# Kernel optimization log

Hardware: AMD Instinct MI355X
Metric: run time of the kernel (lower is better)

Reference implementation:

```python
import jax, jax.numpy as jnp
import numpy as np


def setup_inputs() -> dict:
    key = jax.random.key(0)
    k1, k2 = jax.random.split(key)
    STATE_LEN, SEQ_LEN, D = 8192, 8192, 1024
    user_emb = jax.random.normal(k1, (STATE_LEN, D), dtype=jnp.float32)
    id_emb = jax.random.normal(k2, (SEQ_LEN, D), dtype=jnp.float32)
    return {"user_emb": user_emb, "id_emb": id_emb}


def reference(user_emb, id_emb):
    # attn_energies[i, j] = user_emb[i] . id_emb[j]  -> single GEMM
    energies = jnp.einsum('id,jd->ij', user_emb, id_emb)  # [state_len, seq_len]
    # F.softmax on 2D tensor defaults to dim=1 (rows)
    return jax.nn.softmax(energies, axis=-1)
```

## Files before the change

### kernel.cpp

```cpp
#include <hip/hip_runtime.h>
#include <hip/hip_bf16.h>
#include <stdint.h>

typedef __attribute__((ext_vector_type(8))) short bf16x8;
typedef __attribute__((ext_vector_type(4))) float f32x4;

typedef const __attribute__((address_space(1))) void* gas_ptr;
typedef __attribute__((address_space(3))) void* lds_ptr_t;

__device__ __forceinline__ unsigned short f32_to_bf16_rtn(float x) {
    unsigned u = __float_as_uint(x);
    u += 0x7FFFu + ((u >> 16) & 1u);
    return (unsigned short)(u >> 16);
}
__device__ __forceinline__ float bf16_bits_to_f32(unsigned short h) {
    return __uint_as_float(((unsigned)h) << 16);
}

__global__ __launch_bounds__(256) void split_hi_lo(
    const float* __restrict__ A, const float* __restrict__ B,
    unsigned short* __restrict__ Ahi, unsigned short* __restrict__ Alo,
    unsigned short* __restrict__ Bhi, unsigned short* __restrict__ Blo, int n4)
{
    int i = blockIdx.x * 256 + threadIdx.x;
    if (i >= n4) return;
    float4 a = ((const float4*)A)[i];
    float4 b = ((const float4*)B)[i];
    ushort4 h, l;

    h.x = f32_to_bf16_rtn(a.x); l.x = f32_to_bf16_rtn(a.x - bf16_bits_to_f32(h.x));
    h.y = f32_to_bf16_rtn(a.y); l.y = f32_to_bf16_rtn(a.y - bf16_bits_to_f32(h.y));
    h.z = f32_to_bf16_rtn(a.z); l.z = f32_to_bf16_rtn(a.z - bf16_bits_to_f32(h.z));
    h.w = f32_to_bf16_rtn(a.w); l.w = f32_to_bf16_rtn(a.w - bf16_bits_to_f32(h.w));
    ((ushort4*)Ahi)[i] = h; ((ushort4*)Alo)[i] = l;

    h.x = f32_to_bf16_rtn(b.x); l.x = f32_to_bf16_rtn(b.x - bf16_bits_to_f32(h.x));
    h.y = f32_to_bf16_rtn(b.y); l.y = f32_to_bf16_rtn(b.y - bf16_bits_to_f32(h.y));
    h.z = f32_to_bf16_rtn(b.z); l.z = f32_to_bf16_rtn(b.z - bf16_bits_to_f32(h.z));
    h.w = f32_to_bf16_rtn(b.w); l.w = f32_to_bf16_rtn(b.w - bf16_bits_to_f32(h.w));
    ((ushort4*)Bhi)[i] = h; ((ushort4*)Blo)[i] = l;
}

template<int KC, int NC>
__global__ __launch_bounds__(256) void gemm_presplit(
    const __hip_bfloat16* __restrict__ Ahi, const __hip_bfloat16* __restrict__ Alo,
    const __hip_bfloat16* __restrict__ Bhi, const __hip_bfloat16* __restrict__ Blo,
    float* __restrict__ out, int M, int N, int K)
{
    const int Kd = (KC > 0) ? KC : K;
    const int Nd = (NC > 0) ? NC : N;

    __shared__ char sm[32768];
    const int tid  = threadIdx.x;
    const int lane = tid & 63;
    const int w    = tid >> 6;
    const int bm = blockIdx.y, bn = blockIdx.x;
    const int wm = (w >> 1) * 64;
    const int wn = (w & 1) * 64;

    f32x4 acc[4][4] = {};

    const int sfetch = (tid & 3) ^ ((tid >> 3) & 3);
    const size_t offA = (size_t)(bm * 128 + (tid >> 2)) * Kd + sfetch * 8;
    const size_t offB = (size_t)(bn * 128 + (tid >> 2)) * Kd + sfetch * 8;
    const __hip_bfloat16* pAh = Ahi + offA;
    const __hip_bfloat16* pAl = Alo + offA;
    const __hip_bfloat16* pBh = Bhi + offB;
    const __hip_bfloat16* pBl = Blo + offB;
    const size_t half = (size_t)64 * Kd;
    char* dst0 = sm + tid * 16;

    const int rA = lane & 15;
    const int ca = (lane >> 4) ^ ((lane >> 1) & 3);
    const char* aP = sm +         (wm + rA) * 64 + ca * 16;
    const char* bP = sm + 16384 + (wn + rA) * 64 + ca * 16;

#pragma unroll 4
    for (int k0 = 0; k0 < Kd; k0 += 32) {
        __syncthreads();
        __builtin_amdgcn_global_load_lds((gas_ptr)(pAh + k0),        (lds_ptr_t)(dst0),         16, 0, 0);
        __builtin_amdgcn_global_load_lds((gas_ptr)(pAh + half + k0), (lds_ptr_t)(dst0 + 4096),  16, 0, 0);
        __builtin_amdgcn_global_load_lds((gas_ptr)(pAl + k0),        (lds_ptr_t)(dst0 + 8192),  16, 0, 0);
        __builtin_amdgcn_global_load_lds((gas_ptr)(pAl + half + k0), (lds_ptr_t)(dst0 + 12288), 16, 0, 0);
        __builtin_amdgcn_global_load_lds((gas_ptr)(pBh + k0),        (lds_ptr_t)(dst0 + 16384), 16, 0, 0);
        __builtin_amdgcn_global_load_lds((gas_ptr)(pBh + half + k0), (lds_ptr_t)(dst0 + 20480), 16, 0, 0);
        __builtin_amdgcn_global_load_lds((gas_ptr)(pBl + k0),        (lds_ptr_t)(dst0 + 24576), 16, 0, 0);
        __builtin_amdgcn_global_load_lds((gas_ptr)(pBl + half + k0), (lds_ptr_t)(dst0 + 28672), 16, 0, 0);
        __syncthreads();

        bf16x8 bh[4], bl[4];
#pragma unroll
        for (int j = 0; j < 4; ++j) {
            bh[j] = *(const bf16x8*)(bP + j * 1024);
            bl[j] = *(const bf16x8*)(bP + j * 1024 + 8192);
        }
#pragma unroll
        for (int i = 0; i < 4; ++i) {
            bf16x8 ah = *(const bf16x8*)(aP + i * 1024);
            bf16x8 al = *(const bf16x8*)(aP + i * 1024 + 8192);
#pragma unroll
            for (int j = 0; j < 4; ++j) {
                acc[i][j] = __builtin_amdgcn_mfma_f32_16x16x32_bf16(ah, bh[j], acc[i][j], 0, 0, 0);
                acc[i][j] = __builtin_amdgcn_mfma_f32_16x16x32_bf16(al, bh[j], acc[i][j], 0, 0, 0);
                acc[i][j] = __builtin_amdgcn_mfma_f32_16x16x32_bf16(ah, bl[j], acc[i][j], 0, 0, 0);
            }
        }
    }

    const int r0 = bm * 128 + wm + ((lane >> 4) << 2);
    const int c0 = bn * 128 + wn + rA;
#pragma unroll
    for (int i = 0; i < 4; ++i)
#pragma unroll
        for (int j = 0; j < 4; ++j)
#pragma unroll
            for (int r = 0; r < 4; ++r)
                __builtin_nontemporal_store(
                    acc[i][j][r],
                    &out[(size_t)(r0 + i * 16 + r) * Nd + (c0 + j * 16)]);
}

__global__ __launch_bounds__(256) void gemm_fallback(
    const float* __restrict__ Af, const float* __restrict__ Bf,
    float* __restrict__ out, int M, int N, int K)
{
    __shared__ char sm[32768];
    const int tid  = threadIdx.x;
    const int lane = tid & 63;
    const int w    = tid >> 6;
    const int bm = blockIdx.y, bn = blockIdx.x;
    const int wm = (w >> 1) * 64;
    const int wn = (w & 1) * 64;

    f32x4 acc[4][4] = {};
    const int sfetch = (tid & 3) ^ ((tid >> 3) & 3);
    const int rA = lane & 15;
    const int ca = (lane >> 4) ^ ((lane >> 1) & 3);
    const char* aP = sm +         (wm + rA) * 64 + ca * 16;
    const char* bP = sm + 16384 + (wn + rA) * 64 + ca * 16;

    for (int k0 = 0; k0 < K; k0 += 32) {
        __syncthreads();
#pragma unroll
        for (int c = 0; c < 4; ++c) {
            const bool isA = (c < 2);
            const int row = ((c & 1) << 6) + (tid >> 2);
            const float* src = (isA ? Af + (size_t)(bm * 128 + row) * K
                                    : Bf + (size_t)(bn * 128 + row) * K)
                               + k0 + ((tid & 3) << 3);
            f32x4 v0 = *(const f32x4*)src;
            f32x4 v1 = *(const f32x4*)(src + 4);
            float vv[8] = {v0.x, v0.y, v0.z, v0.w, v1.x, v1.y, v1.z, v1.w};
            bf16x8 h, l;
#pragma unroll
            for (int j = 0; j < 8; ++j) {
                unsigned short hb = f32_to_bf16_rtn(vv[j]);
                unsigned short lb = f32_to_bf16_rtn(vv[j] - bf16_bits_to_f32(hb));
                h[j] = (short)hb; l[j] = (short)lb;
            }
            const int g = row * 64 + sfetch * 16;
            *(bf16x8*)(sm + (isA ? 0 : 16384) + g) = h;
            *(bf16x8*)(sm + (isA ? 8192 : 24576) + g) = l;
        }
        __syncthreads();

        bf16x8 bh[4], bl[4];
#pragma unroll
        for (int j = 0; j < 4; ++j) {
            bh[j] = *(const bf16x8*)(bP + j * 1024);
            bl[j] = *(const bf16x8*)(bP + j * 1024 + 8192);
        }
#pragma unroll
        for (int i = 0; i < 4; ++i) {
            bf16x8 ah = *(const bf16x8*)(aP + i * 1024);
            bf16x8 al = *(const bf16x8*)(aP + i * 1024 + 8192);
#pragma unroll
            for (int j = 0; j < 4; ++j) {
                acc[i][j] = __builtin_amdgcn_mfma_f32_16x16x32_bf16(ah, bh[j], acc[i][j], 0, 0, 0);
                acc[i][j] = __builtin_amdgcn_mfma_f32_16x16x32_bf16(al, bh[j], acc[i][j], 0, 0, 0);
                acc[i][j] = __builtin_amdgcn_mfma_f32_16x16x32_bf16(ah, bl[j], acc[i][j], 0, 0, 0);
            }
        }
    }

    const int r0 = bm * 128 + wm + ((lane >> 4) << 2);
    const int c0 = bn * 128 + wn + rA;
#pragma unroll
    for (int i = 0; i < 4; ++i)
#pragma unroll
        for (int j = 0; j < 4; ++j)
#pragma unroll
            for (int r = 0; r < 4; ++r)
                __builtin_nontemporal_store(
                    acc[i][j][r],
                    &out[(size_t)(r0 + i * 16 + r) * N + (c0 + j * 16)]);
}

__device__ __forceinline__ void lgkm_barrier()
{
    asm volatile("s_waitcnt lgkmcnt(0)" ::: "memory");
    __builtin_amdgcn_s_barrier();
    asm volatile("" ::: "memory");
}

__device__ __forceinline__ void softmax_row(
    f32x4 (&v)[8], f32x4 (&vn)[8], const f32x4* __restrict__ pn, bool pref,
    f32x4* __restrict__ pout, int tid, int slot,
    float (*smax)[4], float (*ssum)[4])
{
    if (pref) {
#pragma unroll
        for (int i = 0; i < 8; ++i) vn[i] = pn[tid + (i << 8)];
    }
    float m = -3.402823466e+38f;
#pragma unroll
    for (int i = 0; i < 8; ++i)
        m = fmaxf(m, fmaxf(fmaxf(v[i].x, v[i].y), fmaxf(v[i].z, v[i].w)));
#pragma unroll
    for (int o = 32; o >= 1; o >>= 1) m = fmaxf(m, __shfl_xor(m, o));
    if ((tid & 63) == 0) smax[slot][tid >> 6] = m;
    lgkm_barrier();
    m = fmaxf(fmaxf(smax[slot][0], smax[slot][1]), fmaxf(smax[slot][2], smax[slot][3]));

    float s = 0.f;
#pragma unroll
    for (int i = 0; i < 8; ++i) {
        v[i].x = __expf(v[i].x - m);
        v[i].y = __expf(v[i].y - m);
        v[i].z = __expf(v[i].z - m);
        v[i].w = __expf(v[i].w - m);
        s += (v[i].x + v[i].y) + (v[i].z + v[i].w);
    }
#pragma unroll
    for (int o = 32; o >= 1; o >>= 1) s += __shfl_xor(s, o);
    if ((tid & 63) == 0) ssum[slot][tid >> 6] = s;
    lgkm_barrier();
    s = (ssum[slot][0] + ssum[slot][1]) + (ssum[slot][2] + ssum[slot][3]);
    const float r = 1.0f / s;
#pragma unroll
    for (int i = 0; i < 8; ++i) {
        v[i] *= r;
        __builtin_nontemporal_store(v[i], &pout[tid + (i << 8)]);
    }
}

__global__ __launch_bounds__(256) void softmax_rows_8192(float* __restrict__ d)
{
    const int tid = threadIdx.x;
    __shared__ float smax[2][4], ssum[2][4];

    f32x4* p0 = (f32x4*)(d + (size_t)blockIdx.x * 4 * 8192);
    f32x4 va[8], vb[8];
#pragma unroll
    for (int i = 0; i < 8; ++i) va[i] = p0[tid + (i << 8)];

    softmax_row(va, vb, p0 + 2048, true,  p0,        tid, 0, smax, ssum);
    softmax_row(vb, va, p0 + 4096, true,  p0 + 2048, tid, 1, smax, ssum);
    softmax_row(va, vb, p0 + 6144, true,  p0 + 4096, tid, 0, smax, ssum);
    softmax_row(vb, va, p0,        false, p0 + 6144, tid, 1, smax, ssum);
}

extern "C" void kernel_launch(void* const* d_in, const int* in_sizes, int n_in,
                              void* d_out, int out_size, void* d_ws, size_t ws_size,
                              hipStream_t stream)
{
    const float* A = (const float*)d_in[0];
    const float* B = (const float*)d_in[1];
    float* out = (float*)d_out;
    const int K = 1024;
    const int M = in_sizes[0] / K;
    const int N = in_sizes[1] / K;
    const size_t elemsA = (size_t)M * K;
    const size_t elemsB = (size_t)N * K;
    const size_t need = 2 * (elemsA + elemsB) * sizeof(unsigned short);

    dim3 grid(N / 128, M / 128);
    const bool presplit = (ws_size >= need) && (M == N);

    if (presplit) {
        unsigned short* Ahi = (unsigned short*)d_ws;
        unsigned short* Alo = Ahi + elemsA;
        unsigned short* Bhi = Alo + elemsA;
        unsigned short* Blo = Bhi + elemsB;
        const int n4 = (int)(elemsA / 4);
        split_hi_lo<<<(n4 + 255) / 256, 256, 0, stream>>>(A, B, Ahi, Alo, Bhi, Blo, n4);
        if (K == 1024 && N == 8192) {
            gemm_presplit<1024, 8192><<<grid, 256, 0, stream>>>(
                (const __hip_bfloat16*)Ahi, (const __hip_bfloat16*)Alo,
                (const __hip_bfloat16*)Bhi, (const __hip_bfloat16*)Blo,
                out, M, N, K);
        } else {
            gemm_presplit<0, 0><<<grid, 256, 0, stream>>>(
                (const __hip_bfloat16*)Ahi, (const __hip_bfloat16*)Alo,
                (const __hip_bfloat16*)Bhi, (const __hip_bfloat16*)Blo,
                out, M, N, K);
        }
    } else {
        gemm_fallback<<<grid, 256, 0, stream>>>(A, B, out, M, N, K);
    }
    softmax_rows_8192<<<M / 4, 256, 0, stream>>>(out);
}
```

Baseline: 731.3 us.

## Double-buffer LDS tiles with vmcnt-based waits in presplit GEMM

Doubles the shared-memory staging buffer to 64KB and software-pipelines the K loop: the next tile's global-to-LDS loads are issued before computing the current tile. Each stage waits only for the older batch of 8 loads (vmcnt(8)) rather than draining everything, and the MFMA section raises wave priority with s_setprio. The aim is to hide global load latency behind MFMA work. In exchange the doubled LDS can reduce how many blocks fit per CU, and the path is now restricted to K divisible by 64.

```diff
diff --git a/kernel.cpp b/kernel.cpp
--- a/kernel.cpp
+++ b/kernel.cpp
@@ -41,6 +41,25 @@
     ((ushort4*)Bhi)[i] = h; ((ushort4*)Blo)[i] = l;
 }
 
+__device__ __forceinline__ void wait_vm8_bar()
+{
+    asm volatile("s_waitcnt vmcnt(8)" ::: "memory");
+    __builtin_amdgcn_s_barrier();
+    asm volatile("" ::: "memory");
+}
+__device__ __forceinline__ void wait_vm0_bar()
+{
+    asm volatile("s_waitcnt vmcnt(0)" ::: "memory");
+    __builtin_amdgcn_s_barrier();
+    asm volatile("" ::: "memory");
+}
+__device__ __forceinline__ void bar_only()
+{
+    asm volatile("" ::: "memory");
+    __builtin_amdgcn_s_barrier();
+    asm volatile("" ::: "memory");
+}
+
 template<int KC, int NC>
 __global__ __launch_bounds__(256) void gemm_presplit(
     const __hip_bfloat16* __restrict__ Ahi, const __hip_bfloat16* __restrict__ Alo,
@@ -50,7 +69,7 @@
     const int Kd = (KC > 0) ? KC : K;
     const int Nd = (NC > 0) ? NC : N;
 
-    __shared__ char sm[32768];
+    __shared__ char sm[65536];
     const int tid  = threadIdx.x;
     const int lane = tid & 63;
     const int w    = tid >> 6;
@@ -75,37 +94,60 @@
     const char* aP = sm +         (wm + rA) * 64 + ca * 16;
     const char* bP = sm + 16384 + (wn + rA) * 64 + ca * 16;
 
-#pragma unroll 4
-    for (int k0 = 0; k0 < Kd; k0 += 32) {
-        __syncthreads();
-        __builtin_amdgcn_global_load_lds((gas_ptr)(pAh + k0),        (lds_ptr_t)(dst0),         16, 0, 0);
-        __builtin_amdgcn_global_load_lds((gas_ptr)(pAh + half + k0), (lds_ptr_t)(dst0 + 4096),  16, 0, 0);
-        __builtin_amdgcn_global_load_lds((gas_ptr)(pAl + k0),        (lds_ptr_t)(dst0 + 8192),  16, 0, 0);
-        __builtin_amdgcn_global_load_lds((gas_ptr)(pAl + half + k0), (lds_ptr_t)(dst0 + 12288), 16, 0, 0);
-        __builtin_amdgcn_global_load_lds((gas_ptr)(pBh + k0),        (lds_ptr_t)(dst0 + 16384), 16, 0, 0);
-        __builtin_amdgcn_global_load_lds((gas_ptr)(pBh + half + k0), (lds_ptr_t)(dst0 + 20480), 16, 0, 0);
-        __builtin_amdgcn_global_load_lds((gas_ptr)(pBl + k0),        (lds_ptr_t)(dst0 + 24576), 16, 0, 0);
-        __builtin_amdgcn_global_load_lds((gas_ptr)(pBl + half + k0), (lds_ptr_t)(dst0 + 28672), 16, 0, 0);
-        __syncthreads();
-
-        bf16x8 bh[4], bl[4];
-#pragma unroll
-        for (int j = 0; j < 4; ++j) {
-            bh[j] = *(const bf16x8*)(bP + j * 1024);
-            bl[j] = *(const bf16x8*)(bP + j * 1024 + 8192);
-        }
-#pragma unroll
-        for (int i = 0; i < 4; ++i) {
-            bf16x8 ah = *(const bf16x8*)(aP + i * 1024);
-            bf16x8 al = *(const bf16x8*)(aP + i * 1024 + 8192);
-#pragma unroll
-            for (int j = 0; j < 4; ++j) {
-                acc[i][j] = __builtin_amdgcn_mfma_f32_16x16x32_bf16(ah, bh[j], acc[i][j], 0, 0, 0);
-                acc[i][j] = __builtin_amdgcn_mfma_f32_16x16x32_bf16(al, bh[j], acc[i][j], 0, 0, 0);
-                acc[i][j] = __builtin_amdgcn_mfma_f32_16x16x32_bf16(ah, bl[j], acc[i][j], 0, 0, 0);
-            }
-        }
-    }
+#define STAGE(BO, kk) do { \
+    __builtin_amdgcn_global_load_lds((gas_ptr)(pAh + (kk)),        (lds_ptr_t)(dst0 + (BO)),          16, 0, 0); \
+    __builtin_amdgcn_global_load_lds((gas_ptr)(pAh + half + (kk)), (lds_ptr_t)(dst0 + (BO) + 4096),   16, 0, 0); \
+    __builtin_amdgcn_global_load_lds((gas_ptr)(pAl + (kk)),        (lds_ptr_t)(dst0 + (BO) + 8192),   16, 0, 0); \
+    __builtin_amdgcn_global_load_lds((gas_ptr)(pAl + half + (kk)), (lds_ptr_t)(dst0 + (BO) + 12288),  16, 0, 0); \
+    __builtin_amdgcn_global_load_lds((gas_ptr)(pBh + (kk)),        (lds_ptr_t)(dst0 + (BO) + 16384),  16, 0, 0); \
+    __builtin_amdgcn_global_load_lds((gas_ptr)(pBh + half + (kk)), (lds_ptr_t)(dst0 + (BO) + 20480),  16, 0, 0); \
+    __builtin_amdgcn_global_load_lds((gas_ptr)(pBl + (kk)),        (lds_ptr_t)(dst0 + (BO) + 24576),  16, 0, 0); \
+    __builtin_amdgcn_global_load_lds((gas_ptr)(pBl + half + (kk)), (lds_ptr_t)(dst0 + (BO) + 28672),  16, 0, 0); \
+} while (0)
+
+#define COMPUTE(BO) do { \
+    bf16x8 bh[4], bl[4]; \
+    _Pragma("unroll") \
+    for (int j = 0; j < 4; ++j) { \
+        bh[j] = *(const bf16x8*)(bP + (BO) + j * 1024); \
+        bl[j] = *(const bf16x8*)(bP + (BO) + j * 1024 + 8192); \
+    } \
+    __builtin_amdgcn_s_setprio(1); \
+    _Pragma("unroll") \
+    for (int i = 0; i < 4; ++i) { \
+        bf16x8 ah = *(const bf16x8*)(aP + (BO) + i * 1024); \
+        bf16x8 al = *(const bf16x8*)(aP + (BO) + i * 1024 + 8192); \
+        _Pragma("unroll") \
+        for (int j = 0; j < 4; ++j) { \
+            acc[i][j] = __builtin_amdgcn_mfma_f32_16x16x32_bf16(ah, bh[j], acc[i][j], 0, 0, 0); \
+            acc[i][j] = __builtin_amdgcn_mfma_f32_16x16x32_bf16(al, bh[j], acc[i][j], 0, 0, 0); \
+            acc[i][j] = __builtin_amdgcn_mfma_f32_16x16x32_bf16(ah, bl[j], acc[i][j], 0, 0, 0); \
+        } \
+    } \
+    __builtin_amdgcn_s_setprio(0); \
+} while (0)
+
+    STAGE(0, 0);
+#pragma unroll 2
+    for (int k0 = 0; k0 < Kd - 64; k0 += 64) {
+        STAGE(32768, k0 + 32);
+        wait_vm8_bar();
+        COMPUTE(0);
+        bar_only();
+        STAGE(0, k0 + 64);
+        wait_vm8_bar();
+        COMPUTE(32768);
+        bar_only();
+    }
+    STAGE(32768, Kd - 32);
+    wait_vm8_bar();
+    COMPUTE(0);
+    bar_only();
+    wait_vm0_bar();
+    COMPUTE(32768);
+
+#undef STAGE
+#undef COMPUTE
 
     const int r0 = bm * 128 + wm + ((lane >> 4) << 2);
     const int c0 = bn * 128 + wn + rA;
@@ -275,7 +317,7 @@
     const size_t need = 2 * (elemsA + elemsB) * sizeof(unsigned short);
 
     dim3 grid(N / 128, M / 128);
-    const bool presplit = (ws_size >= need) && (M == N);
+    const bool presplit = (ws_size >= need) && (M == N) && (K % 64 == 0) && (K >= 128);
 
     if (presplit) {
         unsigned short* Ahi = (unsigned short*)d_ws;
```

Result: no change. 725.1 us (median of 2 runs) (-0.8%).
